# Kernel optimization log

Hardware: AMD Instinct MI355X
Metric: run time of the kernel (lower is better)

Reference implementation:

```python
import jax, jax.numpy as jnp
import numpy as np

N = 4096
INPUT_DIM = 1024
H1 = 512
H2 = 256
NUM_CLASS = 16
ALPHA = 0.2  # leaky relu slope in GAT layers
NEG_INF = -9e15


def _xavier(key, shape, gain=1.414):
    fan_in, fan_out = shape[0], shape[1]
    bound = gain * np.sqrt(6.0 / (fan_in + fan_out))
    return jax.random.uniform(key, shape, jnp.float32, -bound, bound)


def setup_inputs() -> dict:
    key = jax.random.key(0)
    ks = jax.random.split(key, 16)
    X = jax.random.normal(ks[0], (N, INPUT_DIM), jnp.float32)
    Y = jax.random.normal(ks[1], (N, NUM_CLASS), jnp.float32)
    noise = jax.random.normal(ks[2], (N, H2), jnp.float32)
    adj = jax.random.bernoulli(ks[3], 32.0 / N, (N, N))  # bool mask, avg degree ~32
    # GAT layer params: W [in,out], a [2*out,1]
    W0 = _xavier(ks[4], (INPUT_DIM, H1))
    a0 = _xavier(ks[5], (2 * H1, 1))
    W1 = _xavier(ks[6], (H1 + NUM_CLASS, H2))
    a1 = _xavier(ks[7], (2 * H2, 1))
    W2 = _xavier(ks[8], (H1 + NUM_CLASS, H2))
    a2 = _xavier(ks[9], (2 * H2, 1))
    # decoder MLP
    fc1_w = _xavier(ks[10], (H2 + NUM_CLASS, H1), gain=1.0)
    fc1_b = jnp.zeros((H1,), jnp.float32)
    fc2_w = _xavier(ks[11], (H1, N), gain=1.0)
    fc2_b = jnp.zeros((N,), jnp.float32)
    return {"X": X, "Y": Y, "noise": noise, "adj": adj,
            "W0": W0, "a0": a0, "W1": W1, "a1": a1, "W2": W2, "a2": a2,
            "fc1_w": fc1_w, "fc1_b": fc1_b, "fc2_w": fc2_w, "fc2_b": fc2_b}


def gat_layer(x, W, a, adj):
    # Faithful to the torch layer but without materializing [N*N, 2F]:
    # a_input @ a == (h @ a[:F]) broadcast-added to (h @ a[F:]).T
    h = x @ W                       # [N, F]
    F_ = W.shape[1]
    f_src = (h @ a[:F_]).squeeze(-1)  # [N] contribution of row node i
    f_dst = (h @ a[F_:]).squeeze(-1)  # [N] contribution of col node j
    e = jax.nn.leaky_relu(f_src[:, None] + f_dst[None, :], ALPHA)  # [N, N]
    e = jnp.where(adj, e, NEG_INF)
    att = jax.nn.softmax(e, axis=1)  # dropout prob is 0 in this model
    h_prime = att @ h               # [N, F]
    return jax.nn.elu(h_prime)      # concat=True default -> ELU


def reference(X, Y, noise, adj, W0, a0, W1, a1, W2, a2, fc1_w, fc1_b, fc2_w, fc2_b):
    hidden = gat_layer(X, W0, a0, adj)            # [N, H1]
    hidden = jnp.concatenate([hidden, Y], axis=1)  # [N, H1+C]
    mean = gat_layer(hidden, W1, a1, adj)          # [N, H2]
    logstd = gat_layer(hidden, W2, a2, adj)        # [N, H2]
    z = noise * jnp.exp(logstd) + mean             # reparameterization
    z = jnp.concatenate([z, Y], axis=1)            # [N, H2+C]
    z = jax.nn.relu(z @ fc1_w + fc1_b)             # [N, H1]
    A_pred = jax.nn.sigmoid(z @ fc2_w + fc2_b)     # [N, N]
    return A_pred
```

## Files before the change

### kernel.cpp

```cpp
#include <hip/hip_runtime.h>

#define LRELU_ALPHA 0.2f
#define NN 4096
#define CAP 256

typedef unsigned short u16;
typedef short bf16x8 __attribute__((ext_vector_type(8)));
typedef float f32x4 __attribute__((ext_vector_type(4)));
typedef u16 u16x4 __attribute__((ext_vector_type(4)));
typedef u16 u16x2 __attribute__((ext_vector_type(2)));
typedef u16 u16x8 __attribute__((ext_vector_type(8)));

__device__ __forceinline__ u16 f2bf(float f) {
  unsigned u = __float_as_uint(f);
  u += 0x7FFFu + ((u >> 16) & 1u);
  return (u16)(u >> 16);
}
__device__ __forceinline__ float bf2f(u16 u) {
  return __uint_as_float(((unsigned)u) << 16);
}

__device__ __forceinline__ float waveSum(float v) {
  #pragma unroll
  for (int o = 32; o > 0; o >>= 1) v += __shfl_xor(v, o, 64);
  return v;
}
__device__ __forceinline__ float waveMax(float v) {
  #pragma unroll
  for (int o = 32; o > 0; o >>= 1) v = fmaxf(v, __shfl_xor(v, o, 64));
  return v;
}

__device__ __forceinline__ void gload_lds16(const void* g, void* l) {
  __builtin_amdgcn_global_load_lds((const __attribute__((address_space(1))) void*)g,
                                   (__attribute__((address_space(3))) void*)l, 16, 0, 0);
}

__device__ __forceinline__ void lds_barrier() {
  asm volatile("s_waitcnt lgkmcnt(0)" ::: "memory");
  __builtin_amdgcn_s_barrier();
}

__device__ __forceinline__ void csr_body(const unsigned* __restrict__ adjw,
                                         int* __restrict__ nbr, int* __restrict__ cnt,
                                         int i, int* scn)
{
  const int tid = threadIdx.x;
  unsigned bits = 0;
  const unsigned* row = adjw + (size_t)i * 4096 + tid * 16;
  #pragma unroll
  for (int ck = 0; ck < 4; ++ck) {
    uint4 v = *(const uint4*)(row + ck * 4);
    if (v.x) bits |= 1u << (ck * 4 + 0);
    if (v.y) bits |= 1u << (ck * 4 + 1);
    if (v.z) bits |= 1u << (ck * 4 + 2);
    if (v.w) bits |= 1u << (ck * 4 + 3);
  }
  int mycnt = __popc(bits);
  scn[tid] = mycnt;
  __syncthreads();
  for (int off = 1; off < 256; off <<= 1) {
    int v = (tid >= off) ? scn[tid - off] : 0;
    __syncthreads();
    scn[tid] += v;
    __syncthreads();
  }
  const int total = scn[255];
  int pos = scn[tid] - mycnt;
  #pragma unroll
  for (int b = 0; b < 16; ++b) {
    if (bits & (1u << b)) {
      if (pos < CAP) nbr[(size_t)i * CAP + pos] = tid * 16 + b;
      ++pos;
    }
  }
  if (tid == 0) cnt[i] = total;
}

__device__ __forceinline__ void transpose_body(const float* Wsrc, u16* Wt,
                                               int K, int N, int Kpad,
                                               int bx, int by, float (*t)[33]) {
  const int kb = by * 32, nb = bx * 32;
  const int tx = threadIdx.x & 31, ty = threadIdx.x >> 5;
  for (int i = ty; i < 32; i += 8) {
    int k = kb + i, n = nb + tx;
    t[i][tx] = (k < K && n < N) ? Wsrc[(size_t)k * N + n] : 0.f;
  }
  __syncthreads();
  for (int i = ty; i < 32; i += 8) {
    int n = nb + i, k = kb + tx;
    if (n < N && k < Kpad) Wt[(size_t)n * Kpad + k] = f2bf(t[tx][i]);
  }
}

__global__ __launch_bounds__(256) void prep_all(
    const float* __restrict__ W0, u16* __restrict__ W0t,
    const float* __restrict__ W1, u16* __restrict__ W1t,
    const float* __restrict__ W2, u16* __restrict__ W2t,
    const float* __restrict__ fc1w, u16* __restrict__ fc1t,
    const float* __restrict__ X, u16* __restrict__ Xb)
{
  __shared__ float t[32][33];
  const int i = blockIdx.x, tid = threadIdx.x;
  if (i < 512) {
    transpose_body(W0, W0t, 1024, 512, 1024, i & 15, i >> 4, t);
  } else if (i < 656) {
    int j = i - 512;
    transpose_body(W1, W1t, 528, 256, 576, j & 7, j >> 3, t);
  } else if (i < 800) {
    int j = i - 656;
    transpose_body(W2, W2t, 528, 256, 576, j & 7, j >> 3, t);
  } else if (i < 960) {
    int j = i - 800;
    transpose_body(fc1w, fc1t, 272, 512, 320, j & 15, j >> 4, t);
  } else {
    int j = i - 960;
    int idx = j * 256 + tid;
    float4 v = ((const float4*)X)[idx];
    u16x4 o = {f2bf(v.x), f2bf(v.y), f2bf(v.z), f2bf(v.w)};
    ((u16x4*)Xb)[idx] = o;
  }
}

template<int ACT, bool OBF>
__device__ __forceinline__ void gemm64_dev(
    const u16* __restrict__ A, int lda,
    const u16* __restrict__ Bt, int ldb,
    void* __restrict__ Cout, int ldc,
    int K, const float* __restrict__ bias,
    u16 (&As)[2][128 * 64], u16 (&Bs)[2][64 * 64], int bid)
{
  const int tid = threadIdx.x;
  const int lane = tid & 63, wv = tid >> 6;
  const int wm = wv >> 1, wn = wv & 1;
  const int swz = ((bid & 7) << 5) | (bid >> 3);
  const int m0 = (swz >> 3) * 128, n0 = (swz & 7) * 64;
  const int nk = K >> 6;

  f32x4 acc[4][2] = {};

  auto STAGE = [&](int buf, int kt) {
    #pragma unroll
    for (int i = 0; i < 4; ++i) {
      int c = tid + i * 256;
      int r = c >> 3, sl = c & 7;
      int sg = sl ^ (r & 7);
      gload_lds16(A + (size_t)(m0 + r) * lda + kt * 64 + sg * 8, (char*)As[buf] + (c & ~63) * 16);
    }
    #pragma unroll
    for (int i = 0; i < 2; ++i) {
      int c = tid + i * 256;
      int r = c >> 3, sl = c & 7;
      int sg = sl ^ (r & 7);
      gload_lds16(Bt + (size_t)(n0 + r) * ldb + kt * 64 + sg * 8, (char*)Bs[buf] + (c & ~63) * 16);
    }
  };

  STAGE(0, 0);
  if (nk > 1) STAGE(1, 1);

  int cur = 0;
  for (int kt = 0; kt < nk; ++kt) {
    if (kt + 1 < nk) { asm volatile("s_waitcnt vmcnt(6)" ::: "memory"); }
    else             { asm volatile("s_waitcnt vmcnt(0)" ::: "memory"); }
    __builtin_amdgcn_s_barrier();

    #pragma unroll
    for (int ks = 0; ks < 2; ++ks) {
      bf16x8 af[4], bf_[2];
      #pragma unroll
      for (int mi = 0; mi < 4; ++mi) {
        int r = wm * 64 + mi * 16 + (lane & 15);
        int sl = (ks * 4 + (lane >> 4)) ^ (r & 7);
        af[mi] = *(const bf16x8*)((const char*)As[cur] + r * 128 + sl * 16);
      }
      #pragma unroll
      for (int ni = 0; ni < 2; ++ni) {
        int r = wn * 32 + ni * 16 + (lane & 15);
        int sl = (ks * 4 + (lane >> 4)) ^ (r & 7);
        bf_[ni] = *(const bf16x8*)((const char*)Bs[cur] + r * 128 + sl * 16);
      }
      __builtin_amdgcn_s_setprio(1);
      #pragma unroll
      for (int mi = 0; mi < 4; ++mi)
        #pragma unroll
        for (int ni = 0; ni < 2; ++ni)
          acc[mi][ni] = __builtin_amdgcn_mfma_f32_16x16x32_bf16(af[mi], bf_[ni], acc[mi][ni], 0, 0, 0);
      __builtin_amdgcn_s_setprio(0);
    }

    __builtin_amdgcn_s_barrier();
    if (kt + 2 < nk) STAGE(cur, kt + 2);
    cur ^= 1;
  }

  float bv2[2];
  #pragma unroll
  for (int ni = 0; ni < 2; ++ni)
    bv2[ni] = bias ? bias[n0 + wn * 32 + ni * 16 + (lane & 15)] : 0.f;
  float* sc = (float*)As;
  #pragma unroll
  for (int mi = 0; mi < 4; ++mi) {
    lds_barrier();
    const int lr = wm * 16 + (lane >> 4) * 4;
    #pragma unroll
    for (int ni = 0; ni < 2; ++ni) {
      const int lc = wn * 32 + ni * 16 + (lane & 15);
      #pragma unroll
      for (int j = 0; j < 4; ++j) {
        float v = acc[mi][ni][j] + bv2[ni];
        if (ACT == 1) v = fmaxf(v, 0.f);
        if (ACT == 2) v = 1.f / (1.f + __expf(-v));
        sc[(lr + j) * 64 + lc] = v;
      }
    }
    lds_barrier();
    #pragma unroll
    for (int u = 0; u < 2; ++u) {
      int idx = tid + u * 256;
      int r = idx >> 4, c4 = (idx & 15) * 4;
      int grow = m0 + (r >> 4) * 64 + mi * 16 + (r & 15);
      float4 v4 = *(const float4*)(sc + r * 64 + c4);
      if (OBF) {
        u16x4 o = {f2bf(v4.x), f2bf(v4.y), f2bf(v4.z), f2bf(v4.w)};
        *(u16x4*)((u16*)Cout + (size_t)grow * ldc + n0 + c4) = o;
      } else {
        *(float4*)((float*)Cout + (size_t)grow * ldc + n0 + c4) = v4;
      }
    }
  }
}

template<int ACT, bool OBF>
__global__ __launch_bounds__(256) void gemm_mfma64(
    const u16* __restrict__ A, int lda, const u16* __restrict__ Bt, int ldb,
    void* __restrict__ Cout, int ldc, int K, const float* __restrict__ bias)
{
  __shared__ u16 As[2][128 * 64];
  __shared__ u16 Bs[2][64 * 64];
  gemm64_dev<ACT, OBF>(A, lda, Bt, ldb, Cout, ldc, K, bias, As, Bs,
                       blockIdx.y * 8 + blockIdx.x);
}

__global__ __launch_bounds__(256) void csr_gemm0(
    const u16* __restrict__ Xb, const u16* __restrict__ W0t, u16* __restrict__ h0b,
    const unsigned* __restrict__ adjw,
    int* __restrict__ nbr, int* __restrict__ cnt,
    const float* __restrict__ fc2w, u16* __restrict__ fc2t)
{
  __shared__ u16 As[2][128 * 64];
  __shared__ u16 Bs[2][64 * 64];
  if (blockIdx.x < 256) {
    gemm64_dev<0, true>(Xb, 1024, W0t, 1024, h0b, 512, 1024, nullptr, As, Bs, blockIdx.x);
  } else if (blockIdx.x < 4352) {
    csr_body(adjw, nbr, cnt, blockIdx.x - 256, (int*)As);
  } else {
    int j = blockIdx.x - 4352;
    transpose_body(fc2w, fc2t, 512, 4096, 512, j & 127, j >> 7, (float(*)[33])As);
  }
}

__global__ __launch_bounds__(512, 2) void gemm_fc2_8p(
    const u16* __restrict__ A, int lda,
    const u16* __restrict__ Bt, int ldb,
    float* __restrict__ Cout, int ldc,
    int K, const float* __restrict__ bias)
{
  __shared__ u16 As[2][2][128 * 64];
  __shared__ u16 Bs[2][2][128 * 64];
  const int tid = threadIdx.x;
  const int lane = tid & 63, wv = tid >> 6;
  const int wm = wv >> 2, wn = wv & 3;
  const int bid = blockIdx.y * 16 + blockIdx.x;
  const int swz = ((bid & 7) << 5) | (bid >> 3);
  const int m0 = (swz >> 4) * 256, n0 = (swz & 15) * 256;
  const int nk = K >> 6;

  f32x4 acc[8][4] = {};

  auto stA = [&](int slot, int h, int t) {
    const u16* Ap = A + (size_t)(m0 + h * 128) * lda + t * 64;
    #pragma unroll
    for (int i = 0; i < 2; ++i) {
      int c = tid + i * 512;
      int r = c >> 3, sl = c & 7;
      int sg = sl ^ (r & 7);
      gload_lds16(Ap + (size_t)r * lda + sg * 8, (char*)&As[slot][h][0] + (c & ~63) * 16);
    }
  };
  auto stB = [&](int slot, int h, int t) {
    const u16* Bp = Bt + (size_t)(n0 + h * 128) * ldb + t * 64;
    #pragma unroll
    for (int i = 0; i < 2; ++i) {
      int c = tid + i * 512;
      int r = c >> 3, sl = c & 7;
      int sg = sl ^ (r & 7);
      gload_lds16(Bp + (size_t)r * ldb + sg * 8, (char*)&Bs[slot][h][0] + (c & ~63) * 16);
    }
  };

  bf16x8 afl[4][2], afh[4][2], bfl[2][2], bfh[2][2];
  auto rdAq = [&](int slot, int mi0, bf16x8 (&dst)[4][2]) {
    #pragma unroll
    for (int m = 0; m < 4; ++m)
      #pragma unroll
      for (int ks = 0; ks < 2; ++ks) {
        int r = (mi0 + m) * 16 + (lane & 15);
        int sl = (ks * 4 + (lane >> 4)) ^ (r & 7);
        dst[m][ks] = *(const bf16x8*)((const char*)&As[slot][wm][0] + r * 128 + sl * 16);
      }
  };
  auto rdBq = [&](int slot, int ni0, bf16x8 (&dst)[2][2]) {
    #pragma unroll
    for (int n = 0; n < 2; ++n)
      #pragma unroll
      for (int ks = 0; ks < 2; ++ks) {
        int r = (wn & 1) * 64 + (ni0 + n) * 16 + (lane & 15);
        int sl = (ks * 4 + (lane >> 4)) ^ (r & 7);
        dst[n][ks] = *(const bf16x8*)((const char*)&Bs[slot][wn >> 1][0] + r * 128 + sl * 16);
      }
  };
  auto quad = [&](int mi0, int ni0, bf16x8 (&af)[4][2], bf16x8 (&bf)[2][2]) {
    __builtin_amdgcn_s_setprio(1);
    #pragma unroll
    for (int m = 0; m < 4; ++m)
      #pragma unroll
      for (int n = 0; n < 2; ++n)
        #pragma unroll
        for (int ks = 0; ks < 2; ++ks)
          acc[mi0 + m][ni0 + n] =
              __builtin_amdgcn_mfma_f32_16x16x32_bf16(af[m][ks], bf[n][ks], acc[mi0 + m][ni0 + n], 0, 0, 0);
    __builtin_amdgcn_s_setprio(0);
  };
  #define BARX() __builtin_amdgcn_s_barrier()

  stA(0, 0, 0); stA(0, 1, 0); stB(0, 0, 0); stB(0, 1, 0);
  stA(1, 0, 1); stA(1, 1, 1);
  asm volatile("s_waitcnt vmcnt(4)" ::: "memory");
  BARX();

  for (int j = 0; j < nk; j += 2) {
    const bool s2 = (j + 2) < nk;
    rdAq(0, 0, afl); rdBq(0, 0, bfl);
    stB(1, 0, j + 1);
    BARX(); quad(0, 0, afl, bfl); BARX();
    rdAq(0, 4, afh);
    stB(1, 1, j + 1);
    BARX(); quad(4, 0, afh, bfl); BARX();
    rdBq(0, 2, bfh);
    if (s2) stA(0, 0, j + 2);
    BARX(); quad(0, 2, afl, bfh); BARX();
    if (s2) {
      stA(0, 1, j + 2);
      asm volatile("s_waitcnt vmcnt(4)" ::: "memory");
    } else {
      asm volatile("s_waitcnt vmcnt(0)" ::: "memory");
    }
    BARX(); quad(4, 2, afh, bfh); BARX();
    rdAq(1, 0, afl); rdBq(1, 0, bfl);
    if (s2) stB(0, 0, j + 2);
    BARX(); quad(0, 0, afl, bfl); BARX();
    rdAq(1, 4, afh);
    if (s2) stB(0, 1, j + 2);
    BARX(); quad(4, 0, afh, bfl); BARX();
    rdBq(1, 2, bfh);
    if (s2) stA(1, 0, j + 3);
    BARX(); quad(0, 2, afl, bfh); BARX();
    if (s2) {
      stA(1, 1, j + 3);
      asm volatile("s_waitcnt vmcnt(4)" ::: "memory");
    } else {
      asm volatile("s_waitcnt vmcnt(0)" ::: "memory");
    }
    BARX(); quad(4, 2, afh, bfh); BARX();
  }

  float bv4[4];
  #pragma unroll
  for (int ni = 0; ni < 4; ++ni)
    bv4[ni] = bias[n0 + wn * 64 + ni * 16 + (lane & 15)];
  float* sc = (float*)As;
  #pragma unroll
  for (int mi2 = 0; mi2 < 8; mi2 += 2) {
    lds_barrier();
    #pragma unroll
    for (int dm = 0; dm < 2; ++dm) {
      const int mi = mi2 + dm;
      const int lr = wm * 32 + dm * 16 + (lane >> 4) * 4;
      #pragma unroll
      for (int ni = 0; ni < 4; ++ni) {
        const int lc = wn * 64 + ni * 16 + (lane & 15);
        #pragma unroll
        for (int j = 0; j < 4; ++j) {
          float v = acc[mi][ni][j] + bv4[ni];
          v = 1.f / (1.f + __expf(-v));
          sc[(lr + j) * 256 + lc] = v;
        }
      }
    }
    lds_barrier();
    #pragma unroll
    for (int u = 0; u < 8; ++u) {
      int idx = tid + u * 512;
      int r = idx >> 6, c4 = (idx & 63) * 4;
      int grow = m0 + (r >> 5) * 128 + (mi2 + ((r >> 4) & 1)) * 16 + (r & 15);
      f32x4 v4 = *(const f32x4*)(sc + r * 256 + c4);
      __builtin_nontemporal_store(v4, (f32x4*)(Cout + (size_t)grow * ldc + n0 + c4));
    }
  }
}

__global__ __launch_bounds__(256) void fsrc_fdst_bf16(
    const u16* __restrict__ h, const float* __restrict__ a,
    float* __restrict__ fs, float* __restrict__ fd)
{
  const int wid = threadIdx.x >> 6, lane = threadIdx.x & 63;
  const int row = blockIdx.x * 4 + wid;
  u16x8 hv = *(const u16x8*)(h + (size_t)row * 512 + lane * 8);
  float s0 = 0.f, s1 = 0.f;
  #pragma unroll
  for (int j = 0; j < 8; ++j) {
    float x = bf2f(hv[j]);
    s0 = fmaf(x, a[lane * 8 + j], s0);
    s1 = fmaf(x, a[512 + lane * 8 + j], s1);
  }
  s0 = waveSum(s0);
  s1 = waveSum(s1);
  if (lane == 0) { fs[row] = s0; fd[row] = s1; }
}

__global__ __launch_bounds__(256) void fsrc_fdst12_bf16(
    const u16* __restrict__ h12,
    const float* __restrict__ a1, const float* __restrict__ a2,
    float* __restrict__ fs1, float* __restrict__ fd1,
    float* __restrict__ fs2, float* __restrict__ fd2)
{
  const int wid = threadIdx.x >> 6, lane = threadIdx.x & 63;
  const int row = blockIdx.x * 4 + wid;
  u16x8 hv = *(const u16x8*)(h12 + (size_t)row * 512 + lane * 8);
  float s0 = 0.f, s1 = 0.f;
  const bool lo = lane < 32;
  const float* av = lo ? a1 : a2;
  const int base = lo ? lane * 8 : lane * 8 - 256;
  #pragma unroll
  for (int j = 0; j < 8; ++j) {
    float x = bf2f(hv[j]);
    s0 = fmaf(x, av[base + j], s0);
    s1 = fmaf(x, av[256 + base + j], s1);
  }
  #pragma unroll
  for (int o = 16; o > 0; o >>= 1) {
    s0 += __shfl_down(s0, o, 64);
    s1 += __shfl_down(s1, o, 64);
  }
  if (lane == 0)  { fs1[row] = s0; fd1[row] = s1; }
  if (lane == 32) { fs2[row] = s0; fd2[row] = s1; }
}

__global__ __launch_bounds__(256) void agg_gat0(
    const u16* __restrict__ h,
    const float* __restrict__ fs, const float* __restrict__ fd,
    const int* __restrict__ nbr, const int* __restrict__ cnt,
    const float* __restrict__ Y, u16* __restrict__ hb)
{
  __shared__ float2 np[4][CAP];
  const int tid = threadIdx.x;
  const int w = tid >> 6, lane = tid & 63;
  const int r = blockIdx.x * 4 + w;
  int c = cnt[r]; if (c > CAP) c = CAP;
  float acc[8] = {};
  const u16* hp = h + lane * 8;

  if (c > 0) {
    const float fsi = fs[r];
    float e[4];
    int jj[4];
    #pragma unroll
    for (int k = 0; k < 4; ++k) {
      int n = lane + k * 64;
      e[k] = -3.0e38f;
      if (n < c) {
        jj[k] = nbr[(size_t)r * CAP + n];
        float v = fsi + fd[jj[k]];
        e[k] = v > 0.f ? v : LRELU_ALPHA * v;
      }
    }
    float m = waveMax(fmaxf(fmaxf(e[0], e[1]), fmaxf(e[2], e[3])));
    float p[4], ps = 0.f;
    #pragma unroll
    for (int k = 0; k < 4; ++k) {
      int n = lane + k * 64;
      p[k] = (n < c) ? __expf(e[k] - m) : 0.f;
      ps += p[k];
    }
    const float inv = 1.f / waveSum(ps);
    #pragma unroll
    for (int k = 0; k < 4; ++k) {
      int n = lane + k * 64;
      if (n < c) np[w][n] = float2{__int_as_float(jj[k]), p[k] * inv};
    }
    #pragma unroll 4
    for (int n = 0; n < c; ++n) {
      float2 e2 = np[w][n];
      int j = __float_as_int(e2.x);
      float pn = e2.y;
      u16x8 hv = *(const u16x8*)(hp + (size_t)j * 512);
      #pragma unroll
      for (int q = 0; q < 8; ++q) acc[q] = fmaf(pn, bf2f(hv[q]), acc[q]);
    }
  } else {
    for (int j = 0; j < NN; ++j) {
      u16x8 hv = *(const u16x8*)(hp + (size_t)j * 512);
      #pragma unroll
      for (int q = 0; q < 8; ++q) acc[q] += bf2f(hv[q]);
    }
    #pragma unroll
    for (int q = 0; q < 8; ++q) acc[q] *= (1.f / NN);
  }
  u16x8 o;
  #pragma unroll
  for (int q = 0; q < 8; ++q) {
    float v = acc[q] > 0.f ? acc[q] : expm1f(acc[q]);
    o[q] = f2bf(v);
  }
  u16* row = hb + (size_t)r * 576;
  *(u16x8*)(row + lane * 8) = o;
  if (lane < 4) {
    float4 yv = *(const float4*)(Y + (size_t)r * 16 + 4 * lane);
    *(u16x4*)(row + 512 + 4 * lane) = u16x4{f2bf(yv.x), f2bf(yv.y), f2bf(yv.z), f2bf(yv.w)};
  } else if (lane < 16) {
    *(u16x4*)(row + 528 + 4 * (lane - 4)) = u16x4{0, 0, 0, 0};
  }
}

__global__ __launch_bounds__(256) void agg_gat12(
    const u16* __restrict__ h12,
    const float* __restrict__ fs1, const float* __restrict__ fd1,
    const float* __restrict__ fs2, const float* __restrict__ fd2,
    const int* __restrict__ nbr, const int* __restrict__ cnt,
    const float* __restrict__ noise, const float* __restrict__ Y,
    u16* __restrict__ zcat)
{
  __shared__ float4 np[4][CAP];
  const int tid = threadIdx.x;
  const int w = tid >> 6, lane = tid & 63;
  const int r = blockIdx.x * 4 + w;
  int c = cnt[r]; if (c > CAP) c = CAP;
  float acc[8] = {};
  const u16* hp = h12 + lane * 8;

  if (c > 0) {
    const float f1 = fs1[r], f2 = fs2[r];
    float e1[4], e2[4];
    int jj[4];
    #pragma unroll
    for (int k = 0; k < 4; ++k) {
      int n = lane + k * 64;
      e1[k] = -3.0e38f; e2[k] = -3.0e38f;
      if (n < c) {
        jj[k] = nbr[(size_t)r * CAP + n];
        float v1 = f1 + fd1[jj[k]], v2 = f2 + fd2[jj[k]];
        e1[k] = v1 > 0.f ? v1 : LRELU_ALPHA * v1;
        e2[k] = v2 > 0.f ? v2 : LRELU_ALPHA * v2;
      }
    }
    float g1 = waveMax(fmaxf(fmaxf(e1[0], e1[1]), fmaxf(e1[2], e1[3])));
    float g2 = waveMax(fmaxf(fmaxf(e2[0], e2[1]), fmaxf(e2[2], e2[3])));
    float q1[4], q2[4], s1p = 0.f, s2p = 0.f;
    #pragma unroll
    for (int k = 0; k < 4; ++k) {
      int n = lane + k * 64;
      q1[k] = (n < c) ? __expf(e1[k] - g1) : 0.f;
      q2[k] = (n < c) ? __expf(e2[k] - g2) : 0.f;
      s1p += q1[k]; s2p += q2[k];
    }
    const float i1 = 1.f / waveSum(s1p);
    const float i2 = 1.f / waveSum(s2p);
    #pragma unroll
    for (int k = 0; k < 4; ++k) {
      int n = lane + k * 64;
      if (n < c) np[w][n] = float4{__int_as_float(jj[k]), q1[k] * i1, q2[k] * i2, 0.f};
    }
    const bool loHalf = (lane < 32);
    #pragma unroll 4
    for (int n = 0; n < c; ++n) {
      float4 e4 = np[w][n];
      int j = __float_as_int(e4.x);
      float pn = loHalf ? e4.y : e4.z;
      u16x8 hv = *(const u16x8*)(hp + (size_t)j * 512);
      #pragma unroll
      for (int q = 0; q < 8; ++q) acc[q] = fmaf(pn, bf2f(hv[q]), acc[q]);
    }
  } else {
    for (int j = 0; j < NN; ++j) {
      u16x8 hv = *(const u16x8*)(hp + (size_t)j * 512);
      #pragma unroll
      for (int q = 0; q < 8; ++q) acc[q] += bf2f(hv[q]);
    }
    #pragma unroll
    for (int q = 0; q < 8; ++q) acc[q] *= (1.f / NN);
  }
  float v[8];
  #pragma unroll
  for (int q = 0; q < 8; ++q) v[q] = acc[q] > 0.f ? acc[q] : expm1f(acc[q]);
  float lsd[8];
  #pragma unroll
  for (int q = 0; q < 8; ++q) lsd[q] = __shfl_xor(v[q], 32, 64);
  u16* row = zcat + (size_t)r * 320;
  if (lane < 32) {
    const float* nz = noise + (size_t)r * 256 + lane * 8;
    float4 na = *(const float4*)nz, nbv = *(const float4*)(nz + 4);
    float nzv[8] = {na.x, na.y, na.z, na.w, nbv.x, nbv.y, nbv.z, nbv.w};
    u16x8 o;
    #pragma unroll
    for (int q = 0; q < 8; ++q)
      o[q] = f2bf(fmaf(nzv[q], __expf(lsd[q]), v[q]));
    *(u16x8*)(row + lane * 8) = o;
  } else if (lane < 36) {
    float4 yv = *(const float4*)(Y + (size_t)r * 16 + 4 * (lane - 32));
    *(u16x4*)(row + 256 + 4 * (lane - 32)) = u16x4{f2bf(yv.x), f2bf(yv.y), f2bf(yv.z), f2bf(yv.w)};
  } else if (lane < 48) {
    *(u16x4*)(row + 272 + 4 * (lane - 36)) = u16x4{0, 0, 0, 0};
  }
}

extern "C" void kernel_launch(void* const* d_in, const int* in_sizes, int n_in,
                              void* d_out, int out_size, void* d_ws, size_t ws_size,
                              hipStream_t stream)
{
  const float* X     = (const float*)d_in[0];
  const float* Y     = (const float*)d_in[1];
  const float* noise = (const float*)d_in[2];
  const void*  adj   = d_in[3];
  const float* W0    = (const float*)d_in[4];
  const float* a0    = (const float*)d_in[5];
  const float* W1    = (const float*)d_in[6];
  const float* a1    = (const float*)d_in[7];
  const float* W2    = (const float*)d_in[8];
  const float* a2    = (const float*)d_in[9];
  const float* fc1w  = (const float*)d_in[10];
  const float* fc1b  = (const float*)d_in[11];
  const float* fc2w  = (const float*)d_in[12];
  const float* fc2b  = (const float*)d_in[13];
  float* out = (float*)d_out;
  char* W = (char*)d_ws;

  u16*   Xb    = (u16*)(W + 0);
  u16*   zcatb = (u16*)(W + 0);
  u16*   zzb   = (u16*)(W + 2621440);
  u16*   h0b   = (u16*)(W + 8388608);
  u16*   h12b  = (u16*)(W + 8388608);
  u16*   hb    = (u16*)(W + 12582912);
  u16*   W0t   = (u16*)(W + 17301504);
  u16*   W12t  = (u16*)(W + 18350080);
  u16*   fc1t  = (u16*)(W + 18939904);
  u16*   fc2t  = (u16*)(W + 19267584);
  int*   nbr   = (int*)(W + 23461888);
  int*   cnt   = (int*)(W + 27656192);
  float* fs0   = (float*)(W + 27672576);
  float* fd0   = fs0 + 4096;
  float* fs1   = fd0 + 4096;
  float* fd1   = fs1 + 4096;
  float* fs2   = fd1 + 4096;
  float* fd2   = fs2 + 4096;

  prep_all<<<5056, 256, 0, stream>>>(W0, W0t, W1, W12t, W2, W12t + 256 * 576,
                                     fc1w, fc1t, X, Xb);

  csr_gemm0<<<6400, 256, 0, stream>>>(Xb, W0t, h0b, (const unsigned*)adj, nbr, cnt,
                                      fc2w, fc2t);

  fsrc_fdst_bf16<<<1024, 256, 0, stream>>>(h0b, a0, fs0, fd0);
  agg_gat0<<<1024, 256, 0, stream>>>(h0b, fs0, fd0, nbr, cnt, Y, hb);

  gemm_mfma64<0, true><<<dim3(8, 32), 256, 0, stream>>>(hb, 576, W12t, 576, h12b, 512, 576, nullptr);
  fsrc_fdst12_bf16<<<1024, 256, 0, stream>>>(h12b, a1, a2, fs1, fd1, fs2, fd2);
  agg_gat12<<<1024, 256, 0, stream>>>(h12b, fs1, fd1, fs2, fd2, nbr, cnt, noise, Y, zcatb);

  gemm_mfma64<1, true><<<dim3(8, 32), 256, 0, stream>>>(zcatb, 320, fc1t, 320, zzb, 512, 320, fc1b);
  gemm_fc2_8p<<<dim3(16, 16), 512, 0, stream>>>(zzb, 512, fc2t, 512, out, 4096, 512, fc2b);
}
```

Baseline: 116.0 us.

## Fuse attention score projections into GEMM epilogues via atomic accumulation

Computes the per-node f_src/f_dst attention projections inside the GEMM epilogue from the fp32 tile already staged in LDS. Partial sums across column tiles are combined with atomicAdd into buffers that prep_all zero-initialises. This removes the two standalone fsrc_fdst kernels, their re-read of h, and their launch overhead. In exchange it adds atomics and extra LDS reads to the GEMM epilogues. The scores are now computed from fp32 values rather than bf16-rounded ones, and summation order becomes nondeterministic.

```diff
diff --git a/kernel.cpp b/kernel.cpp
--- a/kernel.cpp
+++ b/kernel.cpp
@@ -98,7 +98,8 @@
     const float* __restrict__ W1, u16* __restrict__ W1t,
     const float* __restrict__ W2, u16* __restrict__ W2t,
     const float* __restrict__ fc1w, u16* __restrict__ fc1t,
-    const float* __restrict__ X, u16* __restrict__ Xb)
+    const float* __restrict__ X, u16* __restrict__ Xb,
+    float* __restrict__ fsz)
 {
   __shared__ float t[32][33];
   const int i = blockIdx.x, tid = threadIdx.x;
@@ -113,22 +114,27 @@
   } else if (i < 960) {
     int j = i - 800;
     transpose_body(fc1w, fc1t, 272, 512, 320, j & 15, j >> 4, t);
-  } else {
+  } else if (i < 5056) {
     int j = i - 960;
     int idx = j * 256 + tid;
     float4 v = ((const float4*)X)[idx];
     u16x4 o = {f2bf(v.x), f2bf(v.y), f2bf(v.z), f2bf(v.w)};
     ((u16x4*)Xb)[idx] = o;
-  }
-}
-
-template<int ACT, bool OBF>
+  } else {
+    int j = i - 5056;
+    ((f32x4*)fsz)[j * 256 + tid] = f32x4{0.f, 0.f, 0.f, 0.f};
+  }
+}
+
+template<int ACT, bool OBF, int FS>
 __device__ __forceinline__ void gemm64_dev(
     const u16* __restrict__ A, int lda,
     const u16* __restrict__ Bt, int ldb,
     void* __restrict__ Cout, int ldc,
     int K, const float* __restrict__ bias,
-    u16 (&As)[2][128 * 64], u16 (&Bs)[2][64 * 64], int bid)
+    u16 (&As)[2][128 * 64], u16 (&Bs)[2][64 * 64], int bid,
+    const float* aA, const float* aB,
+    float* fsA, float* fdA, float* fsB, float* fdB)
 {
   const int tid = threadIdx.x;
   const int lane = tid & 63, wv = tid >> 6;
@@ -215,6 +221,36 @@
       }
     }
     lds_barrier();
+    if constexpr (FS > 0) {
+      const float* aS; const float* aD; float* fsO; float* fdO; int colbase;
+      if constexpr (FS == 1) {
+        aS = aA; aD = aA + 512; fsO = fsA; fdO = fdA; colbase = n0;
+      } else {
+        const bool lo2 = (n0 < 256);
+        const float* av = lo2 ? aA : aB;
+        aS = av; aD = av + 256;
+        fsO = lo2 ? fsA : fsB; fdO = lo2 ? fdA : fdB;
+        colbase = n0 & 255;
+      }
+      const int rr = tid >> 3, cg = tid & 7;
+      float s0 = 0.f, s1 = 0.f;
+      #pragma unroll
+      for (int q = 0; q < 8; ++q) {
+        float hv = sc[rr * 64 + cg * 8 + q];
+        s0 = fmaf(hv, aS[colbase + cg * 8 + q], s0);
+        s1 = fmaf(hv, aD[colbase + cg * 8 + q], s1);
+      }
+      #pragma unroll
+      for (int o = 1; o < 8; o <<= 1) {
+        s0 += __shfl_xor(s0, o, 64);
+        s1 += __shfl_xor(s1, o, 64);
+      }
+      if (cg == 0) {
+        int grow = m0 + (rr >> 4) * 64 + mi * 16 + (rr & 15);
+        atomicAdd(fsO + grow, s0);
+        atomicAdd(fdO + grow, s1);
+      }
+    }
     #pragma unroll
     for (int u = 0; u < 2; ++u) {
       int idx = tid + u * 256;
@@ -231,27 +267,31 @@
   }
 }
 
-template<int ACT, bool OBF>
+template<int ACT, bool OBF, int FS>
 __global__ __launch_bounds__(256) void gemm_mfma64(
     const u16* __restrict__ A, int lda, const u16* __restrict__ Bt, int ldb,
-    void* __restrict__ Cout, int ldc, int K, const float* __restrict__ bias)
+    void* __restrict__ Cout, int ldc, int K, const float* __restrict__ bias,
+    const float* aA, const float* aB,
+    float* fsA, float* fdA, float* fsB, float* fdB)
 {
   __shared__ u16 As[2][128 * 64];
   __shared__ u16 Bs[2][64 * 64];
-  gemm64_dev<ACT, OBF>(A, lda, Bt, ldb, Cout, ldc, K, bias, As, Bs,
-                       blockIdx.y * 8 + blockIdx.x);
+  gemm64_dev<ACT, OBF, FS>(A, lda, Bt, ldb, Cout, ldc, K, bias, As, Bs,
+                           blockIdx.y * 8 + blockIdx.x, aA, aB, fsA, fdA, fsB, fdB);
 }
 
 __global__ __launch_bounds__(256) void csr_gemm0(
     const u16* __restrict__ Xb, const u16* __restrict__ W0t, u16* __restrict__ h0b,
     const unsigned* __restrict__ adjw,
     int* __restrict__ nbr, int* __restrict__ cnt,
-    const float* __restrict__ fc2w, u16* __restrict__ fc2t)
+    const float* __restrict__ fc2w, u16* __restrict__ fc2t,
+    const float* __restrict__ a0, float* __restrict__ fs0, float* __restrict__ fd0)
 {
   __shared__ u16 As[2][128 * 64];
   __shared__ u16 Bs[2][64 * 64];
   if (blockIdx.x < 256) {
-    gemm64_dev<0, true>(Xb, 1024, W0t, 1024, h0b, 512, 1024, nullptr, As, Bs, blockIdx.x);
+    gemm64_dev<0, true, 1>(Xb, 1024, W0t, 1024, h0b, 512, 1024, nullptr, As, Bs, blockIdx.x,
+                           a0, nullptr, fs0, fd0, nullptr, nullptr);
   } else if (blockIdx.x < 4352) {
     csr_body(adjw, nbr, cnt, blockIdx.x - 256, (int*)As);
   } else {
@@ -408,53 +448,6 @@
       __builtin_nontemporal_store(v4, (f32x4*)(Cout + (size_t)grow * ldc + n0 + c4));
     }
   }
-}
-
-__global__ __launch_bounds__(256) void fsrc_fdst_bf16(
-    const u16* __restrict__ h, const float* __restrict__ a,
-    float* __restrict__ fs, float* __restrict__ fd)
-{
-  const int wid = threadIdx.x >> 6, lane = threadIdx.x & 63;
-  const int row = blockIdx.x * 4 + wid;
-  u16x8 hv = *(const u16x8*)(h + (size_t)row * 512 + lane * 8);
-  float s0 = 0.f, s1 = 0.f;
-  #pragma unroll
-  for (int j = 0; j < 8; ++j) {
-    float x = bf2f(hv[j]);
-    s0 = fmaf(x, a[lane * 8 + j], s0);
-    s1 = fmaf(x, a[512 + lane * 8 + j], s1);
-  }
-  s0 = waveSum(s0);
-  s1 = waveSum(s1);
-  if (lane == 0) { fs[row] = s0; fd[row] = s1; }
-}
-
-__global__ __launch_bounds__(256) void fsrc_fdst12_bf16(
-    const u16* __restrict__ h12,
-    const float* __restrict__ a1, const float* __restrict__ a2,
-    float* __restrict__ fs1, float* __restrict__ fd1,
-    float* __restrict__ fs2, float* __restrict__ fd2)
-{
-  const int wid = threadIdx.x >> 6, lane = threadIdx.x & 63;
-  const int row = blockIdx.x * 4 + wid;
-  u16x8 hv = *(const u16x8*)(h12 + (size_t)row * 512 + lane * 8);
-  float s0 = 0.f, s1 = 0.f;
-  const bool lo = lane < 32;
-  const float* av = lo ? a1 : a2;
-  const int base = lo ? lane * 8 : lane * 8 - 256;
-  #pragma unroll
-  for (int j = 0; j < 8; ++j) {
-    float x = bf2f(hv[j]);
-    s0 = fmaf(x, av[base + j], s0);
-    s1 = fmaf(x, av[256 + base + j], s1);
-  }
-  #pragma unroll
-  for (int o = 16; o > 0; o >>= 1) {
-    s0 += __shfl_down(s0, o, 64);
-    s1 += __shfl_down(s1, o, 64);
-  }
-  if (lane == 0)  { fs1[row] = s0; fd1[row] = s1; }
-  if (lane == 32) { fs2[row] = s0; fd2[row] = s1; }
 }
 
 __global__ __launch_bounds__(256) void agg_gat0(
@@ -664,19 +657,22 @@
   float* fs2   = fd1 + 4096;
   float* fd2   = fs2 + 4096;
 
-  prep_all<<<5056, 256, 0, stream>>>(W0, W0t, W1, W12t, W2, W12t + 256 * 576,
-                                     fc1w, fc1t, X, Xb);
+  prep_all<<<5080, 256, 0, stream>>>(W0, W0t, W1, W12t, W2, W12t + 256 * 576,
+                                     fc1w, fc1t, X, Xb, fs0);
 
   csr_gemm0<<<6400, 256, 0, stream>>>(Xb, W0t, h0b, (const unsigned*)adj, nbr, cnt,
-                                      fc2w, fc2t);
-
-  fsrc_fdst_bf16<<<1024, 256, 0, stream>>>(h0b, a0, fs0, fd0);
+                                      fc2w, fc2t, a0, fs0, fd0);
+
   agg_gat0<<<1024, 256, 0, stream>>>(h0b, fs0, fd0, nbr, cnt, Y, hb);
 
-  gemm_mfma64<0, true><<<dim3(8, 32), 256, 0, stream>>>(hb, 576, W12t, 576, h12b, 512, 576, nullptr);
-  fsrc_fdst12_bf16<<<1024, 256, 0, stream>>>(h12b, a1, a2, fs1, fd1, fs2, fd2);
+  gemm_mfma64<0, true, 2><<<dim3(8, 32), 256, 0, stream>>>(
+      hb, 576, W12t, 576, h12b, 512, 576, nullptr, a1, a2, fs1, fd1, fs2, fd2);
+
   agg_gat12<<<1024, 256, 0, stream>>>(h12b, fs1, fd1, fs2, fd2, nbr, cnt, noise, Y, zcatb);
 
-  gemm_mfma64<1, true><<<dim3(8, 32), 256, 0, stream>>>(zcatb, 320, fc1t, 320, zzb, 512, 320, fc1b);
+  gemm_mfma64<1, true, 0><<<dim3(8, 32), 256, 0, stream>>>(
+      zcatb, 320, fc1t, 320, zzb, 512, 320, fc1b,
+      nullptr, nullptr, nullptr, nullptr, nullptr, nullptr);
+
   gemm_fc2_8p<<<dim3(16, 16), 512, 0, stream>>>(zzb, 512, fc2t, 512, out, 4096, 512, fc2b);
 }
```

New measurement: 113.0 us. 2.6% less time.
